# Performance work log

Measured on AMD Instinct MI355X. Metric: run time of the kernel, lower is better.

## Reference

```python
import jax, jax.numpy as jnp
import numpy as np


def setup_inputs() -> dict:
    key = jax.random.key(0)
    ks = jax.random.split(key, 14)
    n, c, m, s = 32, 256, 32, 64
    rn = lambda k, shape, sc=1.0: jax.random.normal(k, shape, dtype=jnp.float32) * sc
    return {
        "seg_ori": rn(ks[0], (n, c, m, m)),
        "edge_ori": rn(ks[1], (n, c, m, m)),
        "W_s1": rn(ks[2], (s, c), 0.05), "b_s1": rn(ks[3], (s,), 0.05),
        "W_s11": rn(ks[4], (s, c), 0.05), "b_s11": rn(ks[5], (s,), 0.05),
        "W_mlp": rn(ks[6], (s, c), 0.05), "b_mlp": rn(ks[7], (s,), 0.05),
        "w_s2": rn(ks[8], ()), "b_s2": rn(ks[9], ()),
        "w_s3": rn(ks[10], ()), "b_s3": rn(ks[11], ()),
        "W_g": rn(ks[12], (c, c), 0.02), "b_g": rn(ks[13], (c,), 0.02),
    }


def reference(seg_ori, edge_ori, W_s1, b_s1, W_s11, b_s11, W_mlp, b_mlp,
              w_s2, b_s2, w_s3, b_s3, W_g, b_g):
    n, c, m, _ = seg_ori.shape
    hw = m * m                      # num_n = mids^2
    s = W_s1.shape[0]               # num_s = plane_mid
    seg = seg_ori

    # ---- channel affinity branch ----
    seg_s = jnp.einsum('nchw,sc->nshw', seg, W_s1) + b_s1[None, :, None, None]
    theta_T = seg_s.reshape(n, s, hw)        # view(n, num_s, -1)
    theta = seg_s.reshape(n, hw, s)          # view(n, -1, num_s): reshape, NOT transpose
    ch_att = jax.nn.relu(jnp.mean(seg, axis=(2, 3)) @ W_mlp.T + b_mlp)   # (n, s)
    diag_c = ch_att[:, :, None] * ch_att[:, None, :]                     # (n, s, s) outer
    sim_c = jnp.einsum('nps,nst->npt', theta, diag_c)                    # (n, hw, s)
    sim_c = jax.nn.softmax(jnp.einsum('npt,ntq->npq', sim_c, theta_T), axis=1)  # (n, hw, hw)

    # ---- spatial affinity branch ----
    seg_c = jnp.einsum('nchw,sc->nshw', seg, W_s11) + b_s11[None, :, None, None]
    sigma = seg_c.reshape(n, s, hw)
    sigma_T = seg_c.reshape(n, hw, s)
    sigma_out = jnp.einsum('nps,nsq->npq', sigma_T, sigma)               # (n, hw, hw)
    edge_m = seg * edge_ori
    maxpool_s = jnp.max(seg, axis=1)                                     # (n, m, m)
    edge_m_pool = jnp.max(edge_m, axis=1)                                # (n, m, m)
    seg_ss = (maxpool_s * w_s2 + b_s2).reshape(n, 1, hw)                 # 1x1 conv, 1 channel
    edge_mm = (edge_m_pool * w_s3 + b_s3).reshape(n, hw, 1)
    sim_s = jax.nn.softmax(edge_mm * seg_ss * sigma_out, axis=1)         # (n, hw, hw)

    similarity = sim_c + sim_s

    # ---- GCN: bmm + conv1d(k=1) + relu + residual ----
    seg2 = seg.reshape(n, c, hw)
    seg_sim = jnp.einsum('ncp,npq->ncq', seg2, similarity)               # (n, c, hw)
    out = jax.nn.relu(jnp.einsum('ncl,oc->nol', seg_sim, W_g) + b_g[None, :, None])
    gcn_out = (out + seg2).reshape(n, c, m, m)
    return gcn_out + seg_ori
```

## Files before the change

kernel.cpp:

```cpp
#include <hip/hip_runtime.h>

#define N 32
#define C 256
#define HW 1024
#define S 64
#define LOG2E 1.4426950408889634f

typedef _Float16 f16;
typedef _Float16 f16x4 __attribute__((ext_vector_type(4)));
typedef _Float16 f16x8 __attribute__((ext_vector_type(8)));
typedef float f32x4 __attribute__((ext_vector_type(4)));

#define MFMA(a, b, c) __builtin_amdgcn_mfma_f32_16x16x32_f16(a, b, c, 0, 0, 0)
#define EXP2(x) exp2f(x)

__device__ inline f16x8 lds_ld8(const f16* p) {
    return *(const f16x8*)p;
}

__global__ void __launch_bounds__(256) k_pool1(const float* seg, const float* edge,
        f16* segf, float* pms, float* pme, float* mean,
        const float* Ws1, const float* Ws11, const float* Wg, f16* Wf, f16* Wgf) {
    int n = blockIdx.x, cg = blockIdx.y;
    int t = threadIdx.x, w = t >> 6, lane = t & 63;
    int flat = n * 32 + cg;
    if (flat < 256) {
        int i = flat * 256 + t;
        if (i < S * C) { Wf[i] = (f16)Ws1[i]; Wf[S * C + i] = (f16)Ws11[i]; }
        Wgf[i] = (f16)Wg[i];
    }
    int p4 = (lane << 2) + (w << 8);
    size_t base = (size_t)n * C * HW;
    float4 ms = make_float4(-3e38f, -3e38f, -3e38f, -3e38f);
    float4 me = ms;
    __shared__ float psum[4][8];
    for (int ci = 0; ci < 8; ci++) {
        int c = cg * 8 + ci;
        size_t off = base + (size_t)c * HW + p4;
        float4 s = *(const float4*)(seg + off);
        float4 e = *(const float4*)(edge + off);
        union { f16 h[4]; unsigned long long u; } pk;
        pk.h[0] = (f16)s.x; pk.h[1] = (f16)s.y; pk.h[2] = (f16)s.z; pk.h[3] = (f16)s.w;
        *(unsigned long long*)(segf + off) = pk.u;
        ms.x = fmaxf(ms.x, s.x); ms.y = fmaxf(ms.y, s.y);
        ms.z = fmaxf(ms.z, s.z); ms.w = fmaxf(ms.w, s.w);
        me.x = fmaxf(me.x, s.x * e.x); me.y = fmaxf(me.y, s.y * e.y);
        me.z = fmaxf(me.z, s.z * e.z); me.w = fmaxf(me.w, s.w * e.w);
        float sm = s.x + s.y + s.z + s.w;
        for (int o = 32; o; o >>= 1) sm += __shfl_down(sm, o);
        if (lane == 0) psum[w][ci] = sm;
    }
    __syncthreads();
    if (t < 8)
        mean[n * C + cg * 8 + t] =
            (psum[0][t] + psum[1][t] + psum[2][t] + psum[3][t]) * (1.0f / HW);
    size_t pb = ((size_t)n * 32 + cg) * HW + p4;
    *(float4*)(pms + pb) = ms;
    *(float4*)(pme + pb) = me;
}

__global__ void __launch_bounds__(256) k_pool2(const float* pms, const float* pme,
        float* a2, float* bq, const float* ws2, const float* bs2,
        const float* ws3, const float* bs3,
        const float* mean, const float* Wmlp, const float* bmlp, float* chat) {
    int n = blockIdx.x, t = threadIdx.x;
    int p4 = t << 2;
    float4 ms = make_float4(-3e38f, -3e38f, -3e38f, -3e38f);
    float4 me = ms;
    for (int cg = 0; cg < 32; cg++) {
        size_t pb = ((size_t)n * 32 + cg) * HW + p4;
        float4 a = *(const float4*)(pms + pb);
        float4 b = *(const float4*)(pme + pb);
        ms.x = fmaxf(ms.x, a.x); ms.y = fmaxf(ms.y, a.y);
        ms.z = fmaxf(ms.z, a.z); ms.w = fmaxf(ms.w, a.w);
        me.x = fmaxf(me.x, b.x); me.y = fmaxf(me.y, b.y);
        me.z = fmaxf(me.z, b.z); me.w = fmaxf(me.w, b.w);
    }
    float w3 = ws3[0], b3 = bs3[0], w2 = ws2[0], b2 = bs2[0];
    float4 av, bv;
    av.x = (me.x * w3 + b3) * LOG2E; av.y = (me.y * w3 + b3) * LOG2E;
    av.z = (me.z * w3 + b3) * LOG2E; av.w = (me.w * w3 + b3) * LOG2E;
    bv.x = ms.x * w2 + b2; bv.y = ms.y * w2 + b2;
    bv.z = ms.z * w2 + b2; bv.w = ms.w * w2 + b2;
    *(float4*)(a2 + (size_t)n * HW + p4) = av;
    *(float4*)(bq + (size_t)n * HW + p4) = bv;
    if (t < S) {
        float acc = 0.f;
        const float* wr = Wmlp + (size_t)t * C;
        for (int c = 0; c < C; c++) acc += mean[n * C + c] * wr[c];
        chat[n * S + t] = fmaxf(acc + bmlp[t], 0.f);
    }
}

__global__ void __launch_bounds__(512) k_proj(const f16* segf, const f16* Wf,
        const float* bs1, const float* bs11, const float* chat,
        f16* segc, float* dp2, float* e_, float* dpmm2) {
    int n = blockIdx.x, qt = blockIdx.y;
    int q0 = qt * 64;
    __shared__ f16 sT[64][264];
    __shared__ f16 pT[64][72];
    __shared__ float cA[S];
    const f16* sb = segf + (size_t)n * C * HW + q0;
    int tid = threadIdx.x;
    if (tid < S) cA[tid] = chat[n * S + tid];
    for (int idx = tid; idx < 2048; idx += 512) {
        int c = idx >> 3, q8 = (idx & 7) << 3;
        f16x8 v = *(const f16x8*)(sb + (size_t)c * HW + q8);
        for (int j = 0; j < 8; j++) sT[q8 + j][c] = v[j];
    }
    __syncthreads();
    int lane = tid & 63, wv = tid >> 6;
    int lm = lane & 15, lg = lane >> 4;
    f32x4 acc[4] = {};
    for (int ck = 0; ck < 8; ck++) {
        int c0 = ck * 32;
        f16x8 a0 = *(const f16x8*)(Wf + (size_t)(wv * 16 + lm) * C + c0 + lg * 8);
        for (int j = 0; j < 4; j++) {
            f16x8 b = lds_ld8(&sT[j * 16 + lm][c0 + lg * 8]);
            acc[j] = MFMA(a0, b, acc[j]);
        }
    }
    for (int rr = 0; rr < 4; rr++) {
        int row = wv * 16 + lg * 4 + rr;
        float bias = (row < S) ? bs1[row] : bs11[row - S];
        for (int j = 0; j < 4; j++) {
            int q = q0 + j * 16 + lm;
            float v = acc[j][rr] + bias;
            if (row < S) pT[row][j * 16 + lm] = (f16)v;
            else         segc[((size_t)n * S + (row - S)) * HW + q] = (f16)v;
        }
    }
    __syncthreads();
    if (tid < 64) {
        float a2c = 0.f;
        for (int t = 0; t < S; t += 8) {
            f16x8 v = lds_ld8(&pT[tid][t]);
            for (int j = 0; j < 8; j++) a2c += (float)v[j] * cA[t + j];
        }
        float d2 = a2c * LOG2E;
        dp2[(size_t)n * HW + 16 * tid + qt] = d2;
        float mx = d2, mn = d2;
        for (int o = 32; o; o >>= 1) {
            mx = fmaxf(mx, __shfl_down(mx, o));
            mn = fminf(mn, __shfl_down(mn, o));
        }
        if (tid == 0) {
            dpmm2[(n * 16 + qt) * 2]     = mx;
            dpmm2[(n * 16 + qt) * 2 + 1] = mn;
        }
    } else if (tid < 128) {
        int ql = tid - 64;
        float a2c = 0.f;
        for (int t = 0; t < S; t++) a2c += cA[t] * (float)pT[t][ql];
        e_[(size_t)n * HW + q0 + ql] = a2c;
    }
}

__global__ void __launch_bounds__(256) k_zc(const float* dp2, const float* e_,
        const float* dpmm2, float* Mc2, float* iZc) {
    int n = blockIdx.x, g = blockIdx.y, t = threadIdx.x;
    __shared__ float d[HW];
    for (int i = t; i < HW; i += 256) d[i] = dp2[(size_t)n * HW + i];
    float mx = -3e38f, mn = 3e38f;
    for (int j = 0; j < 16; j++) {
        mx = fmaxf(mx, dpmm2[(n * 16 + j) * 2]);
        mn = fminf(mn, dpmm2[(n * 16 + j) * 2 + 1]);
    }
    __syncthreads();
    int q = g * 32 + (t >> 3);
    int pi = t & 7;
    float eq = e_[(size_t)n * HW + q];
    float m = (eq > 0.f) ? eq * mx : eq * mn;
    float z = 0.f;
    for (int j = 0; j < 128; j++) z += EXP2(d[pi + 8 * j] * eq - m);
    z += __shfl_xor(z, 1);
    z += __shfl_xor(z, 2);
    z += __shfl_xor(z, 4);
    if (pi == 0) {
        Mc2[(size_t)n * HW + q] = m;
        iZc[(size_t)n * HW + q] = 1.f / z;
    }
}

__global__ void __launch_bounds__(512) k_sstats(const f16* segc, const float* a2,
        const float* bq, float* Ms2, float* iZs) {
    int n = blockIdx.x, q0 = blockIdx.y * 32;
    __shared__ f16 bT[32][72];
    __shared__ float a2s[HW];
    __shared__ float mred[32][4], lred[32][4];
    const f16* cb = segc + (size_t)n * S * HW;
    int tid = threadIdx.x;
    if (tid < 256) {
        int th = tid >> 2, q8 = (tid & 3) << 3;
        f16x8 v = *(const f16x8*)(cb + (size_t)th * HW + q0 + q8);
        for (int j = 0; j < 8; j++) bT[q8 + j][th] = v[j];
    }
    for (int i = tid; i < HW; i += 512) a2s[i] = a2[(size_t)n * HW + i];
    __syncthreads();
    int w = tid >> 6, lane = tid & 63, lm = lane & 15, lg = lane >> 4;
    int qg = w >> 2, ph = w & 3;
    f16x8 b0 = lds_ld8(&bT[qg * 16 + lm][lg * 8]);
    f16x8 b1 = lds_ld8(&bT[qg * 16 + lm][32 + lg * 8]);
    float bqv = bq[(size_t)n * HW + q0 + qg * 16 + lm];
    float m = -3e38f, l = 0.f;
    for (int it = 0; it < 8; it++) {
        int pb = ph * 256 + it * 32;
        f16x8 a0 = *(const f16x8*)(cb + (size_t)(pb + lm) * S + lg * 8);
        f16x8 a1 = *(const f16x8*)(cb + (size_t)(pb + lm) * S + 32 + lg * 8);
        f16x8 c0 = *(const f16x8*)(cb + (size_t)(pb + 16 + lm) * S + lg * 8);
        f16x8 c1 = *(const f16x8*)(cb + (size_t)(pb + 16 + lm) * S + 32 + lg * 8);
        f32x4 sgA = {}, sgB = {};
        sgA = MFMA(a0, b0, sgA); sgA = MFMA(a1, b1, sgA);
        sgB = MFMA(c0, b0, sgB); sgB = MFMA(c1, b1, sgB);
        float sc[8];
        float fm = -3e38f;
        for (int rr = 0; rr < 4; rr++) {
            float avA = a2s[pb + lg * 4 + rr];
            float avB = a2s[pb + 16 + lg * 4 + rr];
            sc[rr]     = avA * bqv * sgA[rr];
            sc[rr + 4] = avB * bqv * sgB[rr];
            fm = fmaxf(fm, fmaxf(sc[rr], sc[rr + 4]));
        }
        fm = fmaxf(fm, __shfl_xor(fm, 16));
        fm = fmaxf(fm, __shfl_xor(fm, 32));
        float fl = 0.f;
        for (int rr = 0; rr < 8; rr++) fl += EXP2(sc[rr] - fm);
        fl += __shfl_xor(fl, 16);
        fl += __shfl_xor(fl, 32);
        float nm = fmaxf(m, fm);
        l = l * EXP2(m - nm) + fl * EXP2(fm - nm);
        m = nm;
    }
    if (lg == 0) { mred[qg * 16 + lm][ph] = m; lred[qg * 16 + lm][ph] = l; }
    __syncthreads();
    if (tid < 32) {
        float M = fmaxf(fmaxf(mred[tid][0], mred[tid][1]),
                        fmaxf(mred[tid][2], mred[tid][3]));
        float L = lred[tid][0] * EXP2(mred[tid][0] - M)
                + lred[tid][1] * EXP2(mred[tid][1] - M)
                + lred[tid][2] * EXP2(mred[tid][2] - M)
                + lred[tid][3] * EXP2(mred[tid][3] - M);
        Ms2[(size_t)n * HW + q0 + tid] = M;
        iZs[(size_t)n * HW + q0 + tid] = 1.f / L;
    }
}

__global__ void __launch_bounds__(512, 4) k_fused(const f16* segf, const f16* segc,
        const float* dp2, const float* e_, const float* a2, const float* bq,
        const float* Mc2, const float* iZc, const float* Ms2, const float* iZs,
        const f16* Wgf, const float* bg, float* out) {
    int n = blockIdx.x, q0 = blockIdx.y * 64;
    __shared__ f16 bT[64][72];
    __shared__ f16 wT[2][64][136];
    __shared__ float2 da[HW];
    const f16* cb = segc + (size_t)n * S * HW;
    const f16* sb = segf + (size_t)n * C * HW;
    int tid = threadIdx.x;
    for (int idx = tid; idx < 64 * 32; idx += 512) {
        int q = idx & 63, th = (idx >> 6) << 1;
        union { f16 h[2]; unsigned u; } pk;
        pk.h[0] = cb[(size_t)th * HW + q0 + q];
        pk.h[1] = cb[(size_t)(th + 1) * HW + q0 + q];
        *(unsigned*)&bT[q][th] = pk.u;
    }
    for (int i = tid; i < HW; i += 512)
        da[i] = make_float2(dp2[(size_t)n * HW + i], a2[(size_t)n * HW + i]);
    __syncthreads();
    int w = tid >> 6, lane = tid & 63, lm = lane & 15, lg = lane >> 4;
    float ev[4], bqv[4], mcv[4], izcv[4], msv[4], izsv[4];
    for (int j = 0; j < 4; j++) {
        size_t gq = (size_t)n * HW + q0 + j * 16 + lm;
        ev[j] = e_[gq];  bqv[j] = bq[gq];
        mcv[j] = Mc2[gq]; izcv[j] = iZc[gq];
        msv[j] = Ms2[gq]; izsv[j] = iZs[gq];
    }
    f32x4 acc[2][4] = {};
    for (int chk = 0; chk <= 8; chk++) {
        if (chk > 0) {
            int p0 = (chk - 1) * 128;
            int cur = (chk - 1) & 1;
            #pragma unroll
            for (int ks = 0; ks < 4; ks++) {
                f16x8 a2f[2];
                #pragma unroll
                for (int cf = 0; cf < 2; cf++) {
                    int crow = w * 32 + cf * 16 + lm;
                    a2f[cf] = *(const f16x8*)(sb + (size_t)crow * HW + p0 + ks * 32 + lg * 8);
                }
                #pragma unroll
                for (int qf = 0; qf < 4; qf++) {
                    f16x8 bb = lds_ld8(&wT[cur][qf * 16 + lm][ks * 32 + lg * 8]);
                    acc[0][qf] = MFMA(a2f[0], bb, acc[0][qf]);
                    acc[1][qf] = MFMA(a2f[1], bb, acc[1][qf]);
                }
            }
        }
        if (chk < 8) {
            int p0 = chk * 128;
            const f16* sp = cb + (size_t)(p0 + w * 16 + lm) * S;
            f16x8 sa0 = *(const f16x8*)(sp + lg * 8);
            f16x8 sa1 = *(const f16x8*)(sp + 32 + lg * 8);
            float d2r[4], avr[4];
            #pragma unroll
            for (int rr = 0; rr < 4; rr++) {
                float2 dv = da[p0 + w * 16 + lg * 4 + rr];
                d2r[rr] = dv.x; avr[rr] = dv.y;
            }
            #pragma unroll
            for (int j = 0; j < 4; j++) {
                f16x8 bb0 = lds_ld8(&bT[j * 16 + lm][lg * 8]);
                f16x8 bb1 = lds_ld8(&bT[j * 16 + lm][32 + lg * 8]);
                f32x4 sg = {};
                sg = MFMA(sa0, bb0, sg);
                sg = MFMA(sa1, bb1, sg);
                float wgt[4];
                #pragma unroll
                for (int rr = 0; rr < 4; rr++) {
                    float wc  = EXP2(d2r[rr] * ev[j] - mcv[j]) * izcv[j];
                    float wsv = EXP2(avr[rr] * bqv[j] * sg[rr] - msv[j]) * izsv[j];
                    wgt[rr] = wc + wsv;
                }
                int ql = j * 16 + lm;
                int pp = w * 16 + lg * 4;
                union { f16 h[2]; unsigned u; } c0u, c1u;
                c0u.h[0] = (f16)wgt[0]; c0u.h[1] = (f16)wgt[1];
                c1u.h[0] = (f16)wgt[2]; c1u.h[1] = (f16)wgt[3];
                *(unsigned*)&wT[chk & 1][ql][pp]     = c0u.u;
                *(unsigned*)&wT[chk & 1][ql][pp + 2] = c1u.u;
            }
        }
        __syncthreads();
    }
    f16 (*sT2)[264] = (f16(*)[264])&wT[0][0][0];
    for (int cf = 0; cf < 2; cf++)
        for (int qf = 0; qf < 4; qf++) {
            int crow = w * 32 + cf * 16 + lg * 4;
            int ql = qf * 16 + lm;
            f16x4 pk;
            pk[0] = (f16)acc[cf][qf][0]; pk[1] = (f16)acc[cf][qf][1];
            pk[2] = (f16)acc[cf][qf][2]; pk[3] = (f16)acc[cf][qf][3];
            *(f16x4*)&sT2[ql][crow] = pk;
        }
    __syncthreads();
    int ow = w * 32;
    f32x4 acc2[2][4] = {};
    for (int ck = 0; ck < 8; ck++) {
        int c0 = ck * 32;
        f16x8 af0 = *(const f16x8*)(Wgf + (size_t)(ow + lm) * C + c0 + lg * 8);
        f16x8 af1 = *(const f16x8*)(Wgf + (size_t)(ow + 16 + lm) * C + c0 + lg * 8);
        for (int qf = 0; qf < 4; qf++) {
            f16x8 bf = lds_ld8(&sT2[qf * 16 + lm][c0 + lg * 8]);
            acc2[0][qf] = MFMA(af0, bf, acc2[0][qf]);
            acc2[1][qf] = MFMA(af1, bf, acc2[1][qf]);
        }
    }
    for (int of = 0; of < 2; of++)
        for (int rr = 0; rr < 4; rr++) {
            int o = ow + of * 16 + lg * 4 + rr;
            float bgv = bg[o];
            for (int qf = 0; qf < 4; qf++) {
                int q = q0 + qf * 16 + lm;
                size_t ix = ((size_t)n * C + o) * HW + q;
                out[ix] = fmaxf(acc2[of][qf][rr] + bgv, 0.f) + 2.f * (float)sb[((size_t)o * HW) + q];
            }
        }
}

extern "C" void kernel_launch(void* const* d_in, const int* in_sizes, int n_in,
                              void* d_out, int out_size, void* d_ws, size_t ws_size,
                              hipStream_t stream) {
    const float* seg  = (const float*)d_in[0];
    const float* edge = (const float*)d_in[1];
    const float* Ws1  = (const float*)d_in[2];
    const float* bs1  = (const float*)d_in[3];
    const float* Ws11 = (const float*)d_in[4];
    const float* bs11 = (const float*)d_in[5];
    const float* Wmlp = (const float*)d_in[6];
    const float* bmlp = (const float*)d_in[7];
    const float* ws2  = (const float*)d_in[8];
    const float* bs2  = (const float*)d_in[9];
    const float* ws3  = (const float*)d_in[10];
    const float* bs3  = (const float*)d_in[11];
    const float* Wg   = (const float*)d_in[12];
    const float* bg   = (const float*)d_in[13];
    float* out = (float*)d_out;
    char* wsb = (char*)d_ws;

    f16*   segf   = (f16*)(wsb);
    f16*   segc   = (f16*)(wsb + 16777216);
    float* dpmm2  = (float*)(wsb + 20971520);
    float* pms    = (float*)(wsb + 25165824);
    float* pme    = (float*)(wsb + 29360128);
    f16*   Wf     = (f16*)(wsb + 41943040);
    f16*   Wgf    = (f16*)(wsb + 42008576);
    float* mean   = (float*)(wsb + 42139648);
    float* chat   = (float*)(wsb + 42172416);
    float* dp2    = (float*)(wsb + 42180608);
    float* e_     = (float*)(wsb + 42311680);
    float* a2     = (float*)(wsb + 42442752);
    float* bq     = (float*)(wsb + 42573824);
    float* Mc2    = (float*)(wsb + 42704896);
    float* iZc    = (float*)(wsb + 42835968);
    float* Ms2    = (float*)(wsb + 42967040);
    float* iZs    = (float*)(wsb + 43098112);

    k_pool1<<<dim3(32, 32), 256, 0, stream>>>(seg, edge, segf, pms, pme, mean,
                                              Ws1, Ws11, Wg, Wf, Wgf);
    k_pool2<<<32, 256, 0, stream>>>(pms, pme, a2, bq, ws2, bs2, ws3, bs3,
                                    mean, Wmlp, bmlp, chat);
    k_proj<<<dim3(32, 16), 512, 0, stream>>>(segf, Wf, bs1, bs11, chat,
                                             segc, dp2, e_, dpmm2);
    k_zc<<<dim3(32, 32), 256, 0, stream>>>(dp2, e_, dpmm2, Mc2, iZc);
    k_sstats<<<dim3(32, 32), 512, 0, stream>>>(segc, a2, bq, Ms2, iZs);
    k_fused<<<dim3(32, 16), 512, 0, stream>>>(segf, segc, dp2, e_, a2, bq,
                                              Mc2, iZc, Ms2, iZs, Wgf, bg, out);
}
```

Baseline: 248.3 us.

## Fuse channel-softmax stats into spatial stats kernel and interleave fused-loop MFMA phases

Merges the k_zc kernel, which computes the channel-softmax max and normaliser, into the spatial-stats kernel (now k_zs). The fused kernel loads dp2 into shared memory next to a2 and computes Z with 16 threads per query, which saves one launch and one pass over the inputs. In k_fused the main loop now interleaves, per 32-column step, the aggregation MFMAs for the previous chunk with the weight computation for the next chunk, and hoists the row pointers. The aim is better overlap of global loads, exp work and MFMA, at the cost of extra LDS in the stats kernel and possible register pressure.

Result: no change. 243.5 us (-2.0%).

```diff
diff --git a/kernel.cpp b/kernel.cpp
--- a/kernel.cpp
+++ b/kernel.cpp
@@ -156,37 +156,13 @@
     }
 }
 
-__global__ void __launch_bounds__(256) k_zc(const float* dp2, const float* e_,
-        const float* dpmm2, float* Mc2, float* iZc) {
-    int n = blockIdx.x, g = blockIdx.y, t = threadIdx.x;
-    __shared__ float d[HW];
-    for (int i = t; i < HW; i += 256) d[i] = dp2[(size_t)n * HW + i];
-    float mx = -3e38f, mn = 3e38f;
-    for (int j = 0; j < 16; j++) {
-        mx = fmaxf(mx, dpmm2[(n * 16 + j) * 2]);
-        mn = fminf(mn, dpmm2[(n * 16 + j) * 2 + 1]);
-    }
-    __syncthreads();
-    int q = g * 32 + (t >> 3);
-    int pi = t & 7;
-    float eq = e_[(size_t)n * HW + q];
-    float m = (eq > 0.f) ? eq * mx : eq * mn;
-    float z = 0.f;
-    for (int j = 0; j < 128; j++) z += EXP2(d[pi + 8 * j] * eq - m);
-    z += __shfl_xor(z, 1);
-    z += __shfl_xor(z, 2);
-    z += __shfl_xor(z, 4);
-    if (pi == 0) {
-        Mc2[(size_t)n * HW + q] = m;
-        iZc[(size_t)n * HW + q] = 1.f / z;
-    }
-}
-
-__global__ void __launch_bounds__(512) k_sstats(const f16* segc, const float* a2,
-        const float* bq, float* Ms2, float* iZs) {
+__global__ void __launch_bounds__(512) k_zs(const f16* segc, const float* a2,
+        const float* bq, const float* dp2, const float* e_, const float* dpmm2,
+        float* Ms2, float* iZs, float* Mc2, float* iZc) {
     int n = blockIdx.x, q0 = blockIdx.y * 32;
     __shared__ f16 bT[32][72];
     __shared__ float a2s[HW];
+    __shared__ float d[HW];
     __shared__ float mred[32][4], lred[32][4];
     const f16* cb = segc + (size_t)n * S * HW;
     int tid = threadIdx.x;
@@ -195,7 +171,10 @@
         f16x8 v = *(const f16x8*)(cb + (size_t)th * HW + q0 + q8);
         for (int j = 0; j < 8; j++) bT[q8 + j][th] = v[j];
     }
-    for (int i = tid; i < HW; i += 512) a2s[i] = a2[(size_t)n * HW + i];
+    for (int i = tid; i < HW; i += 512) {
+        a2s[i] = a2[(size_t)n * HW + i];
+        d[i]   = dp2[(size_t)n * HW + i];
+    }
     __syncthreads();
     int w = tid >> 6, lane = tid & 63, lm = lane & 15, lg = lane >> 4;
     int qg = w >> 2, ph = w & 3;
@@ -243,6 +222,25 @@
         Ms2[(size_t)n * HW + q0 + tid] = M;
         iZs[(size_t)n * HW + q0 + tid] = 1.f / L;
     }
+    float mx = -3e38f, mn = 3e38f;
+    for (int j2 = 0; j2 < 16; j2++) {
+        mx = fmaxf(mx, dpmm2[(n * 16 + j2) * 2]);
+        mn = fminf(mn, dpmm2[(n * 16 + j2) * 2 + 1]);
+    }
+    int qz = q0 + (tid >> 4);
+    int pi = tid & 15;
+    float eq = e_[(size_t)n * HW + qz];
+    float mz = (eq > 0.f) ? eq * mx : eq * mn;
+    float z = 0.f;
+    for (int j2 = 0; j2 < 64; j2++) z += EXP2(d[pi + 16 * j2] * eq - mz);
+    z += __shfl_xor(z, 1);
+    z += __shfl_xor(z, 2);
+    z += __shfl_xor(z, 4);
+    z += __shfl_xor(z, 8);
+    if (pi == 0) {
+        Mc2[(size_t)n * HW + qz] = mz;
+        iZc[(size_t)n * HW + qz] = 1.f / z;
+    }
 }
 
 __global__ void __launch_bounds__(512, 4) k_fused(const f16* segf, const f16* segc,
@@ -274,59 +272,57 @@
         mcv[j] = Mc2[gq]; izcv[j] = iZc[gq];
         msv[j] = Ms2[gq]; izsv[j] = iZs[gq];
     }
+    const f16* sbr0 = sb + (size_t)(w * 32 + lm) * HW;
+    const f16* sbr1 = sb + (size_t)(w * 32 + 16 + lm) * HW;
+    const f16* cbr  = cb + (size_t)(w * 16 + lm) * S;
+    int dib = w * 16 + lg * 4;
+    int pp  = w * 16 + lg * 4;
     f32x4 acc[2][4] = {};
     for (int chk = 0; chk <= 8; chk++) {
-        if (chk > 0) {
-            int p0 = (chk - 1) * 128;
-            int cur = (chk - 1) & 1;
+        f16x8 sa0, sa1;
+        float d2r[4], avr[4];
+        if (chk < 8) {
+            const f16* sp = cbr + (size_t)chk * 128 * S;
+            sa0 = *(const f16x8*)(sp + lg * 8);
+            sa1 = *(const f16x8*)(sp + 32 + lg * 8);
             #pragma unroll
-            for (int ks = 0; ks < 4; ks++) {
-                f16x8 a2f[2];
-                #pragma unroll
-                for (int cf = 0; cf < 2; cf++) {
-                    int crow = w * 32 + cf * 16 + lm;
-                    a2f[cf] = *(const f16x8*)(sb + (size_t)crow * HW + p0 + ks * 32 + lg * 8);
-                }
+            for (int rr = 0; rr < 4; rr++) {
+                float2 dv = da[chk * 128 + dib + rr];
+                d2r[rr] = dv.x; avr[rr] = dv.y;
+            }
+        }
+        int p0c = (chk - 1) * 128, cur = (chk - 1) & 1, nxt = chk & 1;
+        #pragma unroll
+        for (int s = 0; s < 4; s++) {
+            if (chk > 0) {
+                f16x8 a0 = *(const f16x8*)(sbr0 + p0c + s * 32 + lg * 8);
+                f16x8 a1 = *(const f16x8*)(sbr1 + p0c + s * 32 + lg * 8);
                 #pragma unroll
                 for (int qf = 0; qf < 4; qf++) {
-                    f16x8 bb = lds_ld8(&wT[cur][qf * 16 + lm][ks * 32 + lg * 8]);
-                    acc[0][qf] = MFMA(a2f[0], bb, acc[0][qf]);
-                    acc[1][qf] = MFMA(a2f[1], bb, acc[1][qf]);
+                    f16x8 bb = lds_ld8(&wT[cur][qf * 16 + lm][s * 32 + lg * 8]);
+                    acc[0][qf] = MFMA(a0, bb, acc[0][qf]);
+                    acc[1][qf] = MFMA(a1, bb, acc[1][qf]);
                 }
             }
-        }
-        if (chk < 8) {
-            int p0 = chk * 128;
-            const f16* sp = cb + (size_t)(p0 + w * 16 + lm) * S;
-            f16x8 sa0 = *(const f16x8*)(sp + lg * 8);
-            f16x8 sa1 = *(const f16x8*)(sp + 32 + lg * 8);
-            float d2r[4], avr[4];
-            #pragma unroll
-            for (int rr = 0; rr < 4; rr++) {
-                float2 dv = da[p0 + w * 16 + lg * 4 + rr];
-                d2r[rr] = dv.x; avr[rr] = dv.y;
-            }
-            #pragma unroll
-            for (int j = 0; j < 4; j++) {
-                f16x8 bb0 = lds_ld8(&bT[j * 16 + lm][lg * 8]);
-                f16x8 bb1 = lds_ld8(&bT[j * 16 + lm][32 + lg * 8]);
+            if (chk < 8) {
+                f16x8 bb0 = lds_ld8(&bT[s * 16 + lm][lg * 8]);
+                f16x8 bb1 = lds_ld8(&bT[s * 16 + lm][32 + lg * 8]);
                 f32x4 sg = {};
                 sg = MFMA(sa0, bb0, sg);
                 sg = MFMA(sa1, bb1, sg);
                 float wgt[4];
                 #pragma unroll
                 for (int rr = 0; rr < 4; rr++) {
-                    float wc  = EXP2(d2r[rr] * ev[j] - mcv[j]) * izcv[j];
-                    float wsv = EXP2(avr[rr] * bqv[j] * sg[rr] - msv[j]) * izsv[j];
+                    float wc  = EXP2(d2r[rr] * ev[s] - mcv[s]) * izcv[s];
+                    float wsv = EXP2(avr[rr] * bqv[s] * sg[rr] - msv[s]) * izsv[s];
                     wgt[rr] = wc + wsv;
                 }
-                int ql = j * 16 + lm;
-                int pp = w * 16 + lg * 4;
+                int ql = s * 16 + lm;
                 union { f16 h[2]; unsigned u; } c0u, c1u;
                 c0u.h[0] = (f16)wgt[0]; c0u.h[1] = (f16)wgt[1];
                 c1u.h[0] = (f16)wgt[2]; c1u.h[1] = (f16)wgt[3];
-                *(unsigned*)&wT[chk & 1][ql][pp]     = c0u.u;
-                *(unsigned*)&wT[chk & 1][ql][pp + 2] = c1u.u;
+                *(unsigned*)&wT[nxt][ql][pp]     = c0u.u;
+                *(unsigned*)&wT[nxt][ql][pp + 2] = c1u.u;
             }
         }
         __syncthreads();
@@ -410,8 +406,8 @@
                                     mean, Wmlp, bmlp, chat);
     k_proj<<<dim3(32, 16), 512, 0, stream>>>(segf, Wf, bs1, bs11, chat,
                                              segc, dp2, e_, dpmm2);
-    k_zc<<<dim3(32, 32), 256, 0, stream>>>(dp2, e_, dpmm2, Mc2, iZc);
-    k_sstats<<<dim3(32, 32), 512, 0, stream>>>(segc, a2, bq, Ms2, iZs);
+    k_zs<<<dim3(32, 32), 512, 0, stream>>>(segc, a2, bq, dp2, e_, dpmm2,
+                                           Ms2, iZs, Mc2, iZc);
     k_fused<<<dim3(32, 16), 512, 0, stream>>>(segf, segc, dp2, e_, a2, bq,
                                               Mc2, iZc, Ms2, iZs, Wgf, bg, out);
 }
```
